# Performance work log

Measured on AMD Instinct MI355X. Metric: run time of the kernel, lower is better.

The kernel has to match this reference:

```python
import jax, jax.numpy as jnp
import numpy as np

K = 7  # window_size from init


def setup_inputs() -> dict:
    key = jax.random.key(0)
    k1, k2, k3 = jax.random.split(key, 3)
    B, S, C, H, W = 2, 5, 256, 200, 200
    hidden = max(C // 16, 4)  # 16
    feats = jax.random.normal(k1, (B, S, C, H, W), dtype=jnp.float32)
    w1 = jax.random.normal(k2, (hidden, C), dtype=jnp.float32) * (1.0 / np.sqrt(C))
    b1 = jnp.zeros((hidden,), dtype=jnp.float32)
    w2 = jax.random.normal(k3, (1, hidden), dtype=jnp.float32) * (1.0 / np.sqrt(hidden))
    b2 = jnp.zeros((1,), dtype=jnp.float32)
    return {"feats": feats, "w1": w1, "b1": b1, "w2": w2, "b2": b2}


def reference(feats, w1, b1, w2, b2):
    B, S, C, H, W = feats.shape
    pad_h = (K - H % K) % K
    pad_w = (K - W % K) % K
    x = jnp.pad(feats, ((0, 0), (0, 0), (0, 0), (0, pad_h), (0, pad_w)))
    Hp, Wp = H + pad_h, W + pad_w
    Hb, Wb = Hp // K, Wp // K
    # windowed view, matching torch unfold(3,k,k).unfold(4,k,k): [B,S,C,Hb,Wb,k,k]
    xw = x.reshape(B, S, C, Hb, K, Wb, K).transpose(0, 1, 2, 3, 5, 4, 6)
    # per-window channel descriptor: mean over the k x k window
    g = xw.mean(axis=(-1, -2))                      # [B,S,C,Hb,Wb]
    g = g.transpose(0, 1, 3, 4, 2)                  # [B,S,Hb,Wb,C]
    h = jax.nn.relu(jnp.einsum('bshwc,dc->bshwd', g, w1) + b1)
    logits = jnp.einsum('bshwd,od->bshwo', h, w2) + b2
    logits = logits[..., 0]                         # [B,S,Hb,Wb]
    # NOTE: faithful to source: softmax over dim=-1 (Wb axis), not the slice axis
    weights = jax.nn.softmax(logits, axis=-1)       # [B,S,Hb,Wb]
    # weighted sum over slices
    fused = jnp.einsum('bschwij,bshw->bchwij', xw, weights)  # [B,C,Hb,Wb,k,k]
    # faithful reassembly: permute(0,1,4,2,5,3) -> [B,C,k,Hb,k,Wb], then reshape
    fused = fused.transpose(0, 1, 4, 2, 5, 3).reshape(B, C, Hp, Wp)
    return fused[:, :, :H, :W]
```

## Files before the change

kernel.cpp:

```cpp
#include <hip/hip_runtime.h>
#include <math.h>

constexpr int B = 2, S = 5, C = 256, H = 200, W = 200;
constexpr int KW = 7;
constexpr int HB = 29, WB = 29;
constexpr int HID = 16;
constexpr int NW = HB * WB;

__global__ __launch_bounds__(512) void k_winsum(const float* __restrict__ feats,
                                                float* __restrict__ gsum) {
    const int blk = (int)blockIdx.x;
    const float* src = feats + (size_t)blk * (H * W);

    __shared__ float colg[HB * W];

    const int tid = (int)threadIdx.x;

    for (int q = tid; q < HB * (W / 4); q += 512) {
        int hb = q / (W / 4);
        int x4 = q - hb * (W / 4);
        int y0 = hb * KW;
        float4 a = make_float4(0.f, 0.f, 0.f, 0.f);
#pragma unroll
        for (int i = 0; i < KW; ++i) {
            int y = y0 + i;
            if (y < H) {
                float4 v = ((const float4*)(src + (size_t)y * W))[x4];
                a.x += v.x; a.y += v.y; a.z += v.z; a.w += v.w;
            }
        }
        ((float4*)(colg + hb * W))[x4] = a;
    }
    __syncthreads();

    float* dst = gsum + (size_t)blk * NW;
    for (int p = tid; p < NW; p += 512) {
        int hb = p / WB;
        int wb = p - hb * WB;
        int x0 = wb * KW;
        float s = 0.f;
#pragma unroll
        for (int j = 0; j < KW; ++j) {
            int x = x0 + j;
            if (x < W) s += colg[hb * W + x];
        }
        dst[p] = s;
    }
}

__global__ __launch_bounds__(256) void k_weights(const float* __restrict__ gsum,
                                                 const float* __restrict__ w1,
                                                 const float* __restrict__ b1,
                                                 const float* __restrict__ w2,
                                                 const float* __restrict__ b2,
                                                 float* __restrict__ weights) {
    int blk = blockIdx.x;
    int hb = blk % HB; blk /= HB;
    int s  = blk % S;
    int b  = blk / S;
    const int bs = b * S + s;

    __shared__ float w1s[HID * C];
    __shared__ float part[8 * HID * WB];
    __shared__ float lg[WB];

    const int tid = (int)threadIdx.x;
    for (int i = tid; i < HID * C; i += 256) w1s[i] = w1[i];
    __syncthreads();

    if (tid < 8 * WB) {
        const int cg = tid / WB;
        const int wb = tid - cg * WB;
        float acc[HID];
#pragma unroll
        for (int d = 0; d < HID; ++d) acc[d] = 0.f;
        const float* g = gsum + (size_t)bs * C * NW + hb * WB + wb;
        const int c0 = cg * (C / 8);
#pragma unroll 4
        for (int c = c0; c < c0 + C / 8; ++c) {
            float gc = g[(size_t)c * NW];
#pragma unroll
            for (int d = 0; d < HID; ++d) acc[d] += gc * w1s[d * C + c];
        }
#pragma unroll
        for (int d = 0; d < HID; ++d) part[(cg * HID + d) * WB + wb] = acc[d];
    }
    __syncthreads();

    if (tid < WB) {
        float logit = b2[0];
#pragma unroll
        for (int d = 0; d < HID; ++d) {
            float a = 0.f;
#pragma unroll
            for (int cg = 0; cg < 8; ++cg) a += part[(cg * HID + d) * WB + tid];
            float h = a * (1.0f / 49.0f) + b1[d];
            logit += fmaxf(h, 0.0f) * w2[d];
        }
        lg[tid] = logit;
    }
    __syncthreads();
    if (tid < WB) {
        float m = -INFINITY;
        for (int t = 0; t < WB; ++t) m = fmaxf(m, lg[t]);
        float sum = 0.f;
        for (int t = 0; t < WB; ++t) sum += expf(lg[t] - m);
        weights[(size_t)bs * NW + hb * WB + tid] = expf(lg[tid] - m) / sum;
    }
}

constexpr int RPB = 4;
__global__ __launch_bounds__(256) void k_fuse(const float* __restrict__ feats,
                                              const float* __restrict__ weights,
                                              float* __restrict__ out) {
    int blk = blockIdx.x;
    const int g = blk % (H / RPB); blk /= (H / RPB);
    const int c = (C - 1) - (blk % C);
    const int b = (B - 1) - (blk / C);
    const int y0 = g * RPB;

    __shared__ float buf[S][RPB][W];
    __shared__ float wsl[S][RPB][WB];

    const int tid = (int)threadIdx.x;
    const size_t plane = (size_t)H * W;
    const size_t sstride = (size_t)C * plane;
    const float* f0 = feats + ((size_t)b * S * C + c) * plane;

    for (int q = tid; q < S * RPB * (W / 4); q += 256) {
        int s  = q / (RPB * (W / 4));
        int r  = q - s * (RPB * (W / 4));
        int yy = r / (W / 4);
        int xq = r - yy * (W / 4);
        int y  = y0 + yy;
        int i  = y / HB;
        int hb = y - i * HB;
        int y_in = hb * KW + i;
        float4 v = make_float4(0.f, 0.f, 0.f, 0.f);
        if (y_in < H)
            v = ((const float4*)(f0 + (size_t)s * sstride + (size_t)y_in * W))[xq];
        ((float4*)&buf[s][yy][0])[xq] = v;
    }
    for (int q = tid; q < S * RPB * 8; q += 256) {
        int s  = q / (RPB * 8);
        int r  = q - s * (RPB * 8);
        int yy = r / 8;
        int f4 = r - yy * 8;
        int hb = (y0 + yy) % HB;
        const float* wrow = weights + ((size_t)((b * S + s) * HB + hb)) * WB;
        float* drow = &wsl[s][yy][0];
        if (f4 < 7) {
            float4 v = make_float4(wrow[f4 * 4], wrow[f4 * 4 + 1],
                                   wrow[f4 * 4 + 2], wrow[f4 * 4 + 3]);
            drow[f4 * 4 + 0] = v.x; drow[f4 * 4 + 1] = v.y;
            drow[f4 * 4 + 2] = v.z; drow[f4 * 4 + 3] = v.w;
        } else {
            drow[28] = wrow[28];
        }
    }
    __syncthreads();

    float* o = out + ((size_t)b * C + c) * plane + (size_t)y0 * W;
    for (int p = tid; p < RPB * (W / 4); p += 256) {
        int yy = p / (W / 4);
        int x0 = (p - yy * (W / 4)) * 4;
        float4 r;
        float* rp = (float*)&r;
#pragma unroll
        for (int u = 0; u < 4; ++u) {
            int x  = x0 + u;
            int j  = x / WB;
            int wb = x - j * WB;
            int x_in = wb * KW + j;
            float acc = 0.f;
            if (x_in < W) {
#pragma unroll
                for (int s = 0; s < S; ++s)
                    acc += buf[s][yy][x_in] * wsl[s][yy][wb];
            }
            rp[u] = acc;
        }
        ((float4*)(o + (size_t)yy * W))[x0 / 4] = r;
    }
}

extern "C" void kernel_launch(void* const* d_in, const int* in_sizes, int n_in,
                              void* d_out, int out_size, void* d_ws, size_t ws_size,
                              hipStream_t stream) {
    const float* feats = (const float*)d_in[0];
    const float* w1    = (const float*)d_in[1];
    const float* b1    = (const float*)d_in[2];
    const float* w2    = (const float*)d_in[3];
    const float* b2    = (const float*)d_in[4];
    float* out = (float*)d_out;

    float* gsum    = (float*)d_ws;
    float* weights = gsum + (size_t)B * S * C * NW;

    hipLaunchKernelGGL(k_winsum, dim3(B * S * C), dim3(512), 0, stream, feats, gsum);
    hipLaunchKernelGGL(k_weights, dim3(B * S * HB), dim3(256), 0, stream,
                       gsum, w1, b1, w2, b2, weights);
    hipLaunchKernelGGL(k_fuse, dim3(B * C * (H / RPB)), dim3(256), 0, stream,
                       feats, weights, out);
}
```

Baseline: 176.3 us.

## Retile fuse kernel per window row so input reads are contiguous

The fuse kernel now assigns one block per (batch, channel, window-row hb) and loads the 7 contiguous input rows of that window strip for each slice. Before, it loaded 4 output rows whose source rows were scattered across the plane. Each block then writes the 7 strided output rows (i*HB+hb) and needs only a single row of softmax weights per slice. The aim is to make global reads contiguous and cut per-element index math and weight loads. The cost is that output writes become strided across rows, and the blocks are larger (512 threads, about 28KB of LDS).

Result: faster. 172.5 us (-2.2%).

```diff
diff --git a/kernel.cpp b/kernel.cpp
--- a/kernel.cpp
+++ b/kernel.cpp
@@ -109,78 +109,63 @@
     }
 }
 
-constexpr int RPB = 4;
-__global__ __launch_bounds__(256) void k_fuse(const float* __restrict__ feats,
+__global__ __launch_bounds__(512) void k_fuse(const float* __restrict__ feats,
                                               const float* __restrict__ weights,
                                               float* __restrict__ out) {
     int blk = blockIdx.x;
-    const int g = blk % (H / RPB); blk /= (H / RPB);
-    const int c = (C - 1) - (blk % C);
-    const int b = (B - 1) - (blk / C);
-    const int y0 = g * RPB;
+    const int hb = blk % HB; blk /= HB;
+    const int c  = (C - 1) - (blk % C);
+    const int b  = (B - 1) - (blk / C);
 
-    __shared__ float buf[S][RPB][W];
-    __shared__ float wsl[S][RPB][WB];
+    __shared__ float buf[S][KW * W];
+    __shared__ float wsl[S][WB];
 
     const int tid = (int)threadIdx.x;
     const size_t plane = (size_t)H * W;
     const size_t sstride = (size_t)C * plane;
     const float* f0 = feats + ((size_t)b * S * C + c) * plane;
+    const int y_in0 = hb * KW;
 
-    for (int q = tid; q < S * RPB * (W / 4); q += 256) {
-        int s  = q / (RPB * (W / 4));
-        int r  = q - s * (RPB * (W / 4));
-        int yy = r / (W / 4);
-        int xq = r - yy * (W / 4);
-        int y  = y0 + yy;
-        int i  = y / HB;
-        int hb = y - i * HB;
-        int y_in = hb * KW + i;
+    for (int q = tid; q < S * 350; q += 512) {
+        int s = q / 350;
+        int r = q - s * 350;
+        int i = r / 50;
         float4 v = make_float4(0.f, 0.f, 0.f, 0.f);
-        if (y_in < H)
-            v = ((const float4*)(f0 + (size_t)s * sstride + (size_t)y_in * W))[xq];
-        ((float4*)&buf[s][yy][0])[xq] = v;
+        if (y_in0 + i < H)
+            v = ((const float4*)(f0 + (size_t)s * sstride + (size_t)y_in0 * W))[r];
+        ((float4*)&buf[s][0])[r] = v;
     }
-    for (int q = tid; q < S * RPB * 8; q += 256) {
-        int s  = q / (RPB * 8);
-        int r  = q - s * (RPB * 8);
-        int yy = r / 8;
-        int f4 = r - yy * 8;
-        int hb = (y0 + yy) % HB;
-        const float* wrow = weights + ((size_t)((b * S + s) * HB + hb)) * WB;
-        float* drow = &wsl[s][yy][0];
-        if (f4 < 7) {
-            float4 v = make_float4(wrow[f4 * 4], wrow[f4 * 4 + 1],
-                                   wrow[f4 * 4 + 2], wrow[f4 * 4 + 3]);
-            drow[f4 * 4 + 0] = v.x; drow[f4 * 4 + 1] = v.y;
-            drow[f4 * 4 + 2] = v.z; drow[f4 * 4 + 3] = v.w;
-        } else {
-            drow[28] = wrow[28];
-        }
+    if (tid < S * WB) {
+        int s  = tid / WB;
+        int wb = tid - s * WB;
+        wsl[s][wb] = weights[((size_t)((b * S + s) * HB + hb)) * WB + wb];
     }
     __syncthreads();
 
-    float* o = out + ((size_t)b * C + c) * plane + (size_t)y0 * W;
-    for (int p = tid; p < RPB * (W / 4); p += 256) {
-        int yy = p / (W / 4);
-        int x0 = (p - yy * (W / 4)) * 4;
-        float4 r;
-        float* rp = (float*)&r;
+    float* o = out + ((size_t)b * C + c) * plane;
+    for (int p = tid; p < KW * 50; p += 512) {
+        int i = p / 50;
+        int y = i * HB + hb;
+        if (y < H) {
+            int x0 = (p - i * 50) * 4;
+            float4 r4;
+            float* rp = (float*)&r4;
 #pragma unroll
-        for (int u = 0; u < 4; ++u) {
-            int x  = x0 + u;
-            int j  = x / WB;
-            int wb = x - j * WB;
-            int x_in = wb * KW + j;
-            float acc = 0.f;
-            if (x_in < W) {
+            for (int u = 0; u < 4; ++u) {
+                int x  = x0 + u;
+                int j  = x / WB;
+                int wb = x - j * WB;
+                int x_in = wb * KW + j;
+                float acc = 0.f;
+                if (x_in < W) {
 #pragma unroll
-                for (int s = 0; s < S; ++s)
-                    acc += buf[s][yy][x_in] * wsl[s][yy][wb];
+                    for (int s = 0; s < S; ++s)
+                        acc += buf[s][i * W + x_in] * wsl[s][wb];
+                }
+                rp[u] = acc;
             }
-            rp[u] = acc;
+            ((float4*)(o + (size_t)y * W))[x0 / 4] = r4;
         }
-        ((float4*)(o + (size_t)yy * W))[x0 / 4] = r;
     }
 }
 
@@ -200,6 +185,6 @@
     hipLaunchKernelGGL(k_winsum, dim3(B * S * C), dim3(512), 0, stream, feats, gsum);
     hipLaunchKernelGGL(k_weights, dim3(B * S * HB), dim3(256), 0, stream,
                        gsum, w1, b1, w2, b2, weights);
-    hipLaunchKernelGGL(k_fuse, dim3(B * C * (H / RPB)), dim3(256), 0, stream,
+    hipLaunchKernelGGL(k_fuse, dim3(B * C * HB), dim3(512), 0, stream,
                        feats, weights, out);
 }
```
